# Kernel optimization log

Measured on AMD Instinct MI355X. Metric: run time of the kernel, lower is better.

Reference implementation:

```python
import jax, jax.numpy as jnp
import numpy as np


def fps(xyz, nsamples):
    # xyz: [B, N, 3] -> [B, nsamples] furthest-point-sample indices (int32)
    def single(p):
        N = p.shape[0]
        def step(carry, _):
            dists, last = carry
            d = jnp.sum((p - p[last]) ** 2, axis=-1)
            dists = jnp.minimum(dists, d)
            return (dists, jnp.argmax(dists).astype(jnp.int32)), last
        init = (jnp.full((N,), 1e10, p.dtype), jnp.int32(0))
        _, idx = jax.lax.scan(step, init, None, length=nsamples)
        return idx
    return jax.vmap(single)(xyz)


def bn_relu(x, g, b, m, v):
    # inference BatchNorm2d folded into scale/shift, then ReLU; x: [B,C,S,N]
    s = g * jax.lax.rsqrt(v + 1e-5)
    return jax.nn.relu(x * s[None, :, None, None] + (b - m * s)[None, :, None, None])


def setup_inputs() -> dict:
    key = jax.random.key(0)
    ks = jax.random.split(key, 6)
    B, N, C, S = 8, 16384, 64, 5
    return dict(
        fg_xyz=jax.random.normal(ks[0], (B, N, 3), jnp.float32),
        fg_features=jax.random.normal(ks[1], (B, C, N), jnp.float32),
        bg_xyz=jax.random.normal(ks[2], (B, N, 3), jnp.float32),
        bg_features=jax.random.normal(ks[3], (B, C, N), jnp.float32),
        w1=jax.random.normal(ks[4], (C, 2 * C), jnp.float32) * (1.0 / np.sqrt(2 * C)),
        g1=jnp.ones((C,), jnp.float32), b1=jnp.zeros((C,), jnp.float32),
        m1=jnp.zeros((C,), jnp.float32), v1=jnp.ones((C,), jnp.float32),
        w2=jax.random.normal(ks[5], (C, C), jnp.float32) * (1.0 / np.sqrt(C)),
        g2=jnp.ones((C,), jnp.float32), b2=jnp.zeros((C,), jnp.float32),
        m2=jnp.zeros((C,), jnp.float32), v2=jnp.ones((C,), jnp.float32),
        nsamples=5,
    )


def reference(fg_xyz, fg_features, bg_xyz, bg_features,
              w1, g1, b1, m1, v1, w2, g2, b2, m2, v2, nsamples):
    B, C, N = fg_features.shape
    S = nsamples
    # D-FPS sample S background points, gather their features: [B, C, S]
    idx = fps(bg_xyz, S)
    sample_bg = jnp.take_along_axis(
        bg_features, jnp.broadcast_to(idx[:, None, :], (B, C, S)), axis=2)
    fg_exp = fg_features[:, :, None, :]                           # [B, C, 1, N]
    # candidates = [fg itself, S sampled bg feats tiled over the N fg points]
    fused_origin = jnp.concatenate(
        [fg_exp, jnp.broadcast_to(sample_bg[:, :, :, None], (B, C, S, N))], axis=2)  # [B,C,S+1,N]
    # weight-net input: fg feature concatenated with each candidate along channels
    fusion_in = jnp.concatenate(
        [jnp.broadcast_to(fg_exp, (B, C, S + 1, N)), fused_origin], axis=1)          # [B,2C,S+1,N]
    h = bn_relu(jnp.einsum('oc,bcsn->bosn', w1, fusion_in), g1, b1, m1, v1)
    w = bn_relu(jnp.einsum('oc,bcsn->bosn', w2, h), g2, b2, m2, v2)                  # [B,C,S+1,N]
    final_feats = jnp.sum(w * fused_origin, axis=2, keepdims=True)                   # [B,C,1,N]
    return fg_xyz, final_feats
```

## Files before the change

kernel.cpp:

```cpp
#include <hip/hip_runtime.h>
#include <hip/hip_bf16.h>

#define B_ 8
#define N_ 16384
#define C_ 64
#define S_ 5

typedef float v4f __attribute__((ext_vector_type(4)));
typedef __bf16 v8bf __attribute__((ext_vector_type(8)));

static __device__ __forceinline__ unsigned short f2bf(float f) {
    unsigned int u = __float_as_uint(f);
    u += 0x7fffu + ((u >> 16) & 1u);
    return (unsigned short)(u >> 16);
}

#define GETF(A, i) (((i) & 3) == 0 ? A[(i) >> 2].x : ((i) & 3) == 1 ? A[(i) >> 2].y \
                    : ((i) & 3) == 2 ? A[(i) >> 2].z : A[(i) >> 2].w)

__global__ __launch_bounds__(1024, 4) void prep_all(
    const float* __restrict__ bg_xyz, const float* __restrict__ bg_feat,
    const float* __restrict__ w1, const float* __restrict__ g1, const float* __restrict__ b1,
    const float* __restrict__ m1, const float* __restrict__ v1,
    const float* __restrict__ w2, const float* __restrict__ g2, const float* __restrict__ b2,
    const float* __restrict__ m2, const float* __restrict__ v2,
    const float* __restrict__ fg_xyz, float* __restrict__ out_xyz,
    float* __restrict__ bb1, float* __restrict__ bb2,
    unsigned short* __restrict__ wa_bf, unsigned short* __restrict__ wc_bf,
    unsigned short* __restrict__ w2_bf,
    float* __restrict__ sbg, float* __restrict__ ebb) {
    const int blk = blockIdx.x;
    const int t = threadIdx.x;

    if (blk >= 9) {
        const int i = (blk - 9) * 1024 + t;
        ((float4*)out_xyz)[i] = ((const float4*)fg_xyz)[i];
        return;
    }

    if (blk == 8) {
        for (int i = t; i < 64 * 64; i += 1024) {
            const int o = i >> 6, c = i & 63;
            const float s1 = g1[o] / sqrtf(v1[o] + 1e-5f);
            const float s2 = g2[o] / sqrtf(v2[o] + 1e-5f);
            const float a = s1 * w1[o * 128 + c];
            const float bbv = s1 * w1[o * 128 + 64 + c];
            wa_bf[o * 64 + c] = f2bf(a);
            wc_bf[o * 64 + c] = f2bf(a + bbv);
            w2_bf[o * 64 + c] = f2bf(s2 * w2[o * 64 + c]);
        }
        if (t < 64) {
            const float s1 = g1[t] / sqrtf(v1[t] + 1e-5f);
            const float s2 = g2[t] / sqrtf(v2[t] + 1e-5f);
            bb1[t] = b1[t] - m1[t] * s1;
            bb2[t] = b2[t] - m2[t] * s2;
        }
        return;
    }

    const int b = blk;
    const float* p = bg_xyz + (size_t)b * N_ * 3;

    float4 f4[12];
    {
        const float4* pv = (const float4*)p + t * 12;
#pragma unroll
        for (int i = 0; i < 12; ++i) f4[i] = pv[i];
    }
    float px[16], py[16], pz[16], dist[16];
#pragma unroll
    for (int k = 0; k < 16; ++k) {
        px[k] = GETF(f4, 3 * k);
        py[k] = GETF(f4, 3 * k + 1);
        pz[k] = GETF(f4, 3 * k + 2);
        dist[k] = 1e10f;
    }

    __shared__ float s_best[16];
    __shared__ int s_bidx[16];
    __shared__ int s_last;
    __shared__ int s_idx[S_];
    __shared__ float sf[S_][64];
    int last = 0;
    if (t == 0) s_idx[0] = 0;

    for (int step = 1; step < S_; ++step) {
        const float lx = p[last * 3 + 0];
        const float ly = p[last * 3 + 1];
        const float lz = p[last * 3 + 2];
        float best = -1.0f;
        int bidx = 0;
#pragma unroll
        for (int k = 0; k < 16; ++k) {
            float dx = px[k] - lx, dy = py[k] - ly, dz = pz[k] - lz;
            float d = dx * dx + dy * dy + dz * dz;
            float nd = fminf(dist[k], d);
            dist[k] = nd;
            if (nd > best) { best = nd; bidx = t * 16 + k; }
        }
#pragma unroll
        for (int off = 32; off > 0; off >>= 1) {
            float ob = __shfl_down(best, off, 64);
            int oi = __shfl_down(bidx, off, 64);
            if (ob > best || (ob == best && oi < bidx)) { best = ob; bidx = oi; }
        }
        if ((t & 63) == 0) { s_best[t >> 6] = best; s_bidx[t >> 6] = bidx; }
        __syncthreads();
        if (t == 0) {
            float bb = s_best[0];
            int bi = s_bidx[0];
#pragma unroll
            for (int w = 1; w < 16; ++w) {
                if (s_best[w] > bb || (s_best[w] == bb && s_bidx[w] < bi)) {
                    bb = s_best[w];
                    bi = s_bidx[w];
                }
            }
            s_last = bi;
            s_idx[step] = bi;
        }
        __syncthreads();
        last = s_last;
        __syncthreads();
    }

    __syncthreads();
    if (t < S_ * 64) {
        const int j = t >> 6, c = t & 63;
        sf[j][c] = bg_feat[(size_t)b * C_ * N_ + (size_t)c * N_ + s_idx[j]];
    }
    __syncthreads();
    if (t < S_ * 64) {
        const int j = t >> 6, o = t & 63;
        const float s1 = g1[o] * rsqrtf(v1[o] + 1e-5f);
        const float4* wr = (const float4*)&w1[o * 128 + 64];
        float acc = 0.f;
#pragma unroll
        for (int c4 = 0; c4 < 16; ++c4) {
            float4 wv = wr[c4];
            acc += wv.x * sf[j][c4 * 4 + 0] + wv.y * sf[j][c4 * 4 + 1] +
                   wv.z * sf[j][c4 * 4 + 2] + wv.w * sf[j][c4 * 4 + 3];
        }
        sbg[(b * S_ + j) * 64 + o] = sf[j][o];
        ebb[(b * S_ + j) * 64 + o] = s1 * acc + (b1[o] - m1[o] * s1);
    }
}

#define FP 64
#define HP 72

__global__ __launch_bounds__(256) void fusion_main(
    const float* __restrict__ fg_feat,
    const unsigned short* __restrict__ wa_bf, const unsigned short* __restrict__ wc_bf,
    const unsigned short* __restrict__ w2_bf,
    const float* __restrict__ bb1g, const float* __restrict__ bb2g,
    const float* __restrict__ ebbg, const float* __restrict__ sbgg,
    float* __restrict__ out) {
    __shared__ __align__(16) float Flds[64 * FP];
    __shared__ __align__(16) unsigned short Ht[2][4][16 * HP];
    __shared__ __align__(16) float cEbb[S_ * 64];
    __shared__ __align__(16) float cSbg[S_ * 64];
    __shared__ __align__(16) float cBb1[64];
    __shared__ __align__(16) float cBb2[64];

    const int t = threadIdx.x;
    const int b = blockIdx.y;
    const int n0 = blockIdx.x * 64;
    const float* Fg = fg_feat + (size_t)b * C_ * N_ + n0;

    const int lane = t & 63;
    const int w = t >> 6;

    {
        const int crow = lane >> 4;
        const int nq = lane & 15;
#pragma unroll
        for (int r = 0; r < 4; ++r) {
            const int c = r * 16 + w * 4;
            const float* gsrc = Fg + (size_t)(c + crow) * N_ + nq * 4;
            __builtin_amdgcn_global_load_lds(
                (const __attribute__((address_space(1))) unsigned int*)gsrc,
                (__attribute__((address_space(3))) unsigned int*)&Flds[c * FP],
                16, 0, 0);
        }
    }

    for (int i = t; i < S_ * 64; i += 256) {
        cEbb[i] = ebbg[b * (S_ * 64) + i];
        cSbg[i] = sbgg[b * (S_ * 64) + i];
    }
    if (t < 64) { cBb1[t] = bb1g[t]; cBb2[t] = bb2g[t]; }

    const int m = lane & 15;
    const int q = lane >> 4;
    const int nrow = w * 16 + m;

    v8bf aW2[4][2];
#pragma unroll
    for (int ob = 0; ob < 4; ++ob)
#pragma unroll
        for (int ks = 0; ks < 2; ++ks)
            aW2[ob][ks] = *(const v8bf*)&w2_bf[(ob * 16 + m) * 64 + ks * 32 + q * 8];

    __syncthreads();

    v8bf bF[2];
#pragma unroll
    for (int ks = 0; ks < 2; ++ks) {
        unsigned int uu[4];
#pragma unroll
        for (int jp = 0; jp < 4; ++jp) {
            const int c = ks * 32 + q * 8 + jp * 2;
            float2 fp2;
            fp2.x = Flds[c * FP + nrow];
            fp2.y = Flds[(c + 1) * FP + nrow];
            __hip_bfloat162 h2 = __float22bfloat162_rn(fp2);
            __builtin_memcpy(&uu[jp], &h2, 4);
        }
        __builtin_memcpy(&bF[ks], uu, 16);
    }

    v4f U[4], U0[4];
#pragma unroll
    for (int ob = 0; ob < 4; ++ob) {
        v8bf a0 = *(const v8bf*)&wa_bf[(ob * 16 + m) * 64 + q * 8];
        v8bf a1 = *(const v8bf*)&wa_bf[(ob * 16 + m) * 64 + 32 + q * 8];
        v4f z = {0.f, 0.f, 0.f, 0.f};
        z = __builtin_amdgcn_mfma_f32_16x16x32_bf16(a0, bF[0], z, 0, 0, 0);
        U[ob] = __builtin_amdgcn_mfma_f32_16x16x32_bf16(a1, bF[1], z, 0, 0, 0);
        v8bf c0 = *(const v8bf*)&wc_bf[(ob * 16 + m) * 64 + q * 8];
        v8bf c1 = *(const v8bf*)&wc_bf[(ob * 16 + m) * 64 + 32 + q * 8];
        v4f z2 = {0.f, 0.f, 0.f, 0.f};
        z2 = __builtin_amdgcn_mfma_f32_16x16x32_bf16(c0, bF[0], z2, 0, 0, 0);
        U0[ob] = __builtin_amdgcn_mfma_f32_16x16x32_bf16(c1, bF[1], z2, 0, 0, 0);
    }

    v4f acc[4];
#pragma unroll
    for (int ob = 0; ob < 4; ++ob) acc[ob] = (v4f){0.f, 0.f, 0.f, 0.f};

#pragma unroll
    for (int s = 0; s < 6; ++s) {
        unsigned short* h = &Ht[s & 1][w][0];

#pragma unroll
        for (int ob = 0; ob < 4; ++ob) {
            const int o4 = ob * 16 + 4 * q;
            v4f u, cv;
            if (s == 0) { u = U0[ob]; cv = *(const v4f*)&cBb1[o4]; }
            else        { u = U[ob];  cv = *(const v4f*)&cEbb[(s - 1) * 64 + o4]; }
            float2 e01, e23;
            e01.x = fmaxf(u[0] + cv[0], 0.f);
            e01.y = fmaxf(u[1] + cv[1], 0.f);
            e23.x = fmaxf(u[2] + cv[2], 0.f);
            e23.y = fmaxf(u[3] + cv[3], 0.f);
            __hip_bfloat162 h01 = __float22bfloat162_rn(e01);
            __hip_bfloat162 h23 = __float22bfloat162_rn(e23);
            unsigned int lo, hi;
            __builtin_memcpy(&lo, &h01, 4);
            __builtin_memcpy(&hi, &h23, 4);
            unsigned long long vv = (unsigned long long)lo | ((unsigned long long)hi << 32);
            *(unsigned long long*)&h[m * HP + o4] = vv;
        }

        v8bf hb0 = *(const v8bf*)&h[m * HP + q * 8];
        v8bf hb1 = *(const v8bf*)&h[m * HP + 32 + q * 8];

#pragma unroll
        for (int ob = 0; ob < 4; ++ob) {
            v4f z = {0.f, 0.f, 0.f, 0.f};
            z = __builtin_amdgcn_mfma_f32_16x16x32_bf16(aW2[ob][0], hb0, z, 0, 0, 0);
            v4f p4 = __builtin_amdgcn_mfma_f32_16x16x32_bf16(aW2[ob][1], hb1, z, 0, 0, 0);

            const int o4 = ob * 16 + 4 * q;
            const v4f b2v = *(const v4f*)&cBb2[o4];
            if (s == 0) {
#pragma unroll
                for (int r = 0; r < 4; ++r) {
                    float wgt = fmaxf(p4[r] + b2v[r], 0.f);
                    acc[ob][r] += wgt * Flds[(o4 + r) * FP + nrow];
                }
            } else {
                const v4f sb = *(const v4f*)&cSbg[(s - 1) * 64 + o4];
#pragma unroll
                for (int r = 0; r < 4; ++r) {
                    float wgt = fmaxf(p4[r] + b2v[r], 0.f);
                    acc[ob][r] += wgt * sb[r];
                }
            }
        }
    }

#pragma unroll
    for (int ob = 0; ob < 4; ++ob)
#pragma unroll
        for (int r = 0; r < 4; ++r)
            out[(size_t)b * C_ * N_ + (size_t)(ob * 16 + 4 * q + r) * N_ + (n0 + w * 16 + m)] =
                acc[ob][r];
}

extern "C" void kernel_launch(void* const* d_in, const int* in_sizes, int n_in,
                              void* d_out, int out_size, void* d_ws, size_t ws_size,
                              hipStream_t stream) {
    const float* fg_xyz = (const float*)d_in[0];
    const float* fg_feat = (const float*)d_in[1];
    const float* bg_xyz = (const float*)d_in[2];
    const float* bg_feat = (const float*)d_in[3];
    const float* w1 = (const float*)d_in[4];
    const float* g1 = (const float*)d_in[5];
    const float* b1 = (const float*)d_in[6];
    const float* m1 = (const float*)d_in[7];
    const float* v1 = (const float*)d_in[8];
    const float* w2 = (const float*)d_in[9];
    const float* g2 = (const float*)d_in[10];
    const float* b2 = (const float*)d_in[11];
    const float* m2 = (const float*)d_in[12];
    const float* v2 = (const float*)d_in[13];

    float* ws = (float*)d_ws;
    float* ebb = ws;
    float* sbg = ebb + 2560;
    float* bb1 = sbg + 2560;
    float* bb2 = bb1 + 64;
    unsigned short* wa_bf = (unsigned short*)(bb2 + 64);
    unsigned short* wc_bf = wa_bf + 4096;
    unsigned short* w2_bf = wc_bf + 4096;

    float* out_feats = (float*)d_out + (size_t)B_ * N_ * 3;

    prep_all<<<105, 1024, 0, stream>>>(bg_xyz, bg_feat,
                                       w1, g1, b1, m1, v1, w2, g2, b2, m2, v2,
                                       fg_xyz, (float*)d_out,
                                       bb1, bb2, wa_bf, wc_bf, w2_bf, sbg, ebb);
    fusion_main<<<dim3(N_ / 64, B_), 256, 0, stream>>>(
        fg_feat, wa_bf, wc_bf, w2_bf, bb1, bb2, ebb, sbg, out_feats);
}
```

Before: 178.0 us.

## Process two tiles per block, prefetch second tile, split output channels across waves

Each block now handles two 64-point tiles, and the global loads for the second tile are issued before the first tile is computed. Work is split across waves by output-channel slice rather than point slice, so each wave keeps only its own weight fragments in registers. Features are stored in shared memory as bf16 in a transposed, padded layout, and the fg term in the weighted sum now uses the bf16 values. The cost is block-wide barriers inside each of the six candidate iterations, a halved grid, and slightly lower precision on the fg feature product.

```diff
diff --git a/kernel.cpp b/kernel.cpp
--- a/kernel.cpp
+++ b/kernel.cpp
@@ -8,11 +8,15 @@
 
 typedef float v4f __attribute__((ext_vector_type(4)));
 typedef __bf16 v8bf __attribute__((ext_vector_type(8)));
+typedef unsigned int v4u __attribute__((ext_vector_type(4)));
 
 static __device__ __forceinline__ unsigned short f2bf(float f) {
     unsigned int u = __float_as_uint(f);
     u += 0x7fffu + ((u >> 16) & 1u);
     return (unsigned short)(u >> 16);
+}
+static __device__ __forceinline__ float bf2f(unsigned short s) {
+    return __uint_as_float(((unsigned int)s) << 16);
 }
 
 #define GETF(A, i) (((i) & 3) == 0 ? A[(i) >> 2].x : ((i) & 3) == 1 ? A[(i) >> 2].y \
@@ -146,18 +150,17 @@
     }
 }
 
-#define FP 64
-#define HP 72
-
-__global__ __launch_bounds__(256) void fusion_main(
+#define PITCH 72
+
+__global__ __launch_bounds__(256, 4) void fusion_main(
     const float* __restrict__ fg_feat,
     const unsigned short* __restrict__ wa_bf, const unsigned short* __restrict__ wc_bf,
     const unsigned short* __restrict__ w2_bf,
     const float* __restrict__ bb1g, const float* __restrict__ bb2g,
     const float* __restrict__ ebbg, const float* __restrict__ sbgg,
     float* __restrict__ out) {
-    __shared__ __align__(16) float Flds[64 * FP];
-    __shared__ __align__(16) unsigned short Ht[2][4][16 * HP];
+    __shared__ __align__(16) unsigned short Ft[2][64 * PITCH];
+    __shared__ __align__(16) unsigned short Ht[64 * PITCH];
     __shared__ __align__(16) float cEbb[S_ * 64];
     __shared__ __align__(16) float cSbg[S_ * 64];
     __shared__ __align__(16) float cBb1[64];
@@ -165,25 +168,8 @@
 
     const int t = threadIdx.x;
     const int b = blockIdx.y;
-    const int n0 = blockIdx.x * 64;
-    const float* Fg = fg_feat + (size_t)b * C_ * N_ + n0;
-
-    const int lane = t & 63;
-    const int w = t >> 6;
-
-    {
-        const int crow = lane >> 4;
-        const int nq = lane & 15;
-#pragma unroll
-        for (int r = 0; r < 4; ++r) {
-            const int c = r * 16 + w * 4;
-            const float* gsrc = Fg + (size_t)(c + crow) * N_ + nq * 4;
-            __builtin_amdgcn_global_load_lds(
-                (const __attribute__((address_space(1))) unsigned int*)gsrc,
-                (__attribute__((address_space(3))) unsigned int*)&Flds[c * FP],
-                16, 0, 0);
-        }
-    }
+    const float* Fbase = fg_feat + (size_t)b * C_ * N_;
+    const size_t outb = (size_t)b * C_ * N_;
 
     for (int i = t; i < S_ * 64; i += 256) {
         cEbb[i] = ebbg[b * (S_ * 64) + i];
@@ -191,112 +177,151 @@
     }
     if (t < 64) { cBb1[t] = bb1g[t]; cBb2[t] = bb2g[t]; }
 
+    const int lane = t & 63;
+    const int wv = t >> 6;
+    const int o0 = wv * 16;
     const int m = lane & 15;
     const int q = lane >> 4;
-    const int nrow = w * 16 + m;
-
-    v8bf aW2[4][2];
-#pragma unroll
-    for (int ob = 0; ob < 4; ++ob)
-#pragma unroll
-        for (int ks = 0; ks < 2; ++ks)
-            aW2[ob][ks] = *(const v8bf*)&w2_bf[(ob * 16 + m) * 64 + ks * 32 + q * 8];
-
+    const int o4 = o0 + 4 * q;
+
+    const int arow = o0 + m;
+    v8bf aWa[2], aWc[2], aW2[2];
+#pragma unroll
+    for (int ks = 0; ks < 2; ++ks) {
+        aWa[ks] = *(const v8bf*)&wa_bf[arow * 64 + ks * 32 + q * 8];
+        aWc[ks] = *(const v8bf*)&wc_bf[arow * 64 + ks * 32 + q * 8];
+        aW2[ks] = *(const v8bf*)&w2_bf[arow * 64 + ks * 32 + q * 8];
+    }
+
+    const int sn = t & 63;
+    const int cg = (t >> 6) * 16;
+
+    {
+        const float* Fg = Fbase + (size_t)blockIdx.x * 64 + sn;
+        float fr[16];
+#pragma unroll
+        for (int i = 0; i < 16; ++i) fr[i] = Fg[(size_t)(cg + i) * N_];
+        v4u w0, w1v;
+#pragma unroll
+        for (int i = 0; i < 8; ++i) {
+            unsigned int pk = (unsigned int)f2bf(fr[2 * i]) |
+                              ((unsigned int)f2bf(fr[2 * i + 1]) << 16);
+            if (i < 4) w0[i] = pk; else w1v[i - 4] = pk;
+        }
+        *(v4u*)&Ft[0][sn * PITCH + cg] = w0;
+        *(v4u*)&Ft[0][sn * PITCH + cg + 8] = w1v;
+    }
     __syncthreads();
 
-    v8bf bF[2];
-#pragma unroll
-    for (int ks = 0; ks < 2; ++ks) {
-        unsigned int uu[4];
-#pragma unroll
-        for (int jp = 0; jp < 4; ++jp) {
-            const int c = ks * 32 + q * 8 + jp * 2;
-            float2 fp2;
-            fp2.x = Flds[c * FP + nrow];
-            fp2.y = Flds[(c + 1) * FP + nrow];
-            __hip_bfloat162 h2 = __float22bfloat162_rn(fp2);
-            __builtin_memcpy(&uu[jp], &h2, 4);
-        }
-        __builtin_memcpy(&bF[ks], uu, 16);
-    }
-
-    v4f U[4], U0[4];
-#pragma unroll
-    for (int ob = 0; ob < 4; ++ob) {
-        v8bf a0 = *(const v8bf*)&wa_bf[(ob * 16 + m) * 64 + q * 8];
-        v8bf a1 = *(const v8bf*)&wa_bf[(ob * 16 + m) * 64 + 32 + q * 8];
-        v4f z = {0.f, 0.f, 0.f, 0.f};
-        z = __builtin_amdgcn_mfma_f32_16x16x32_bf16(a0, bF[0], z, 0, 0, 0);
-        U[ob] = __builtin_amdgcn_mfma_f32_16x16x32_bf16(a1, bF[1], z, 0, 0, 0);
-        v8bf c0 = *(const v8bf*)&wc_bf[(ob * 16 + m) * 64 + q * 8];
-        v8bf c1 = *(const v8bf*)&wc_bf[(ob * 16 + m) * 64 + 32 + q * 8];
-        v4f z2 = {0.f, 0.f, 0.f, 0.f};
-        z2 = __builtin_amdgcn_mfma_f32_16x16x32_bf16(c0, bF[0], z2, 0, 0, 0);
-        U0[ob] = __builtin_amdgcn_mfma_f32_16x16x32_bf16(c1, bF[1], z2, 0, 0, 0);
-    }
-
-    v4f acc[4];
-#pragma unroll
-    for (int ob = 0; ob < 4; ++ob) acc[ob] = (v4f){0.f, 0.f, 0.f, 0.f};
-
-#pragma unroll
-    for (int s = 0; s < 6; ++s) {
-        unsigned short* h = &Ht[s & 1][w][0];
-
-#pragma unroll
-        for (int ob = 0; ob < 4; ++ob) {
-            const int o4 = ob * 16 + 4 * q;
-            v4f u, cv;
-            if (s == 0) { u = U0[ob]; cv = *(const v4f*)&cBb1[o4]; }
-            else        { u = U[ob];  cv = *(const v4f*)&cEbb[(s - 1) * 64 + o4]; }
-            float2 e01, e23;
-            e01.x = fmaxf(u[0] + cv[0], 0.f);
-            e01.y = fmaxf(u[1] + cv[1], 0.f);
-            e23.x = fmaxf(u[2] + cv[2], 0.f);
-            e23.y = fmaxf(u[3] + cv[3], 0.f);
-            __hip_bfloat162 h01 = __float22bfloat162_rn(e01);
-            __hip_bfloat162 h23 = __float22bfloat162_rn(e23);
-            unsigned int lo, hi;
-            __builtin_memcpy(&lo, &h01, 4);
-            __builtin_memcpy(&hi, &h23, 4);
-            unsigned long long vv = (unsigned long long)lo | ((unsigned long long)hi << 32);
-            *(unsigned long long*)&h[m * HP + o4] = vv;
-        }
-
-        v8bf hb0 = *(const v8bf*)&h[m * HP + q * 8];
-        v8bf hb1 = *(const v8bf*)&h[m * HP + 32 + q * 8];
-
-#pragma unroll
-        for (int ob = 0; ob < 4; ++ob) {
+    float fr1[16];
+    {
+        const float* Fg1 = Fbase + (size_t)(blockIdx.x + 128) * 64 + sn;
+#pragma unroll
+        for (int i = 0; i < 16; ++i) fr1[i] = Fg1[(size_t)(cg + i) * N_];
+    }
+
+    const v4f bb1r = *(const v4f*)&cBb1[o4];
+    const v4f bb2r = *(const v4f*)&cBb2[o4];
+
+    auto tile_compute = [&](const unsigned short* F, size_t obase) {
+        v8bf bF[4][2];
+#pragma unroll
+        for (int nb = 0; nb < 4; ++nb)
+#pragma unroll
+            for (int ks = 0; ks < 2; ++ks)
+                bF[nb][ks] = *(const v8bf*)&F[(nb * 16 + m) * PITCH + ks * 32 + q * 8];
+
+        v4f U[4], U0[4];
+#pragma unroll
+        for (int nb = 0; nb < 4; ++nb) {
             v4f z = {0.f, 0.f, 0.f, 0.f};
-            z = __builtin_amdgcn_mfma_f32_16x16x32_bf16(aW2[ob][0], hb0, z, 0, 0, 0);
-            v4f p4 = __builtin_amdgcn_mfma_f32_16x16x32_bf16(aW2[ob][1], hb1, z, 0, 0, 0);
-
-            const int o4 = ob * 16 + 4 * q;
-            const v4f b2v = *(const v4f*)&cBb2[o4];
-            if (s == 0) {
-#pragma unroll
-                for (int r = 0; r < 4; ++r) {
-                    float wgt = fmaxf(p4[r] + b2v[r], 0.f);
-                    acc[ob][r] += wgt * Flds[(o4 + r) * FP + nrow];
-                }
-            } else {
-                const v4f sb = *(const v4f*)&cSbg[(s - 1) * 64 + o4];
-#pragma unroll
-                for (int r = 0; r < 4; ++r) {
-                    float wgt = fmaxf(p4[r] + b2v[r], 0.f);
-                    acc[ob][r] += wgt * sb[r];
+            z = __builtin_amdgcn_mfma_f32_16x16x32_bf16(aWa[0], bF[nb][0], z, 0, 0, 0);
+            U[nb] = __builtin_amdgcn_mfma_f32_16x16x32_bf16(aWa[1], bF[nb][1], z, 0, 0, 0);
+            v4f z2 = {0.f, 0.f, 0.f, 0.f};
+            z2 = __builtin_amdgcn_mfma_f32_16x16x32_bf16(aWc[0], bF[nb][0], z2, 0, 0, 0);
+            U0[nb] = __builtin_amdgcn_mfma_f32_16x16x32_bf16(aWc[1], bF[nb][1], z2, 0, 0, 0);
+        }
+
+        v4f acc[4];
+#pragma unroll
+        for (int nb = 0; nb < 4; ++nb) acc[nb] = (v4f){0.f, 0.f, 0.f, 0.f};
+
+#pragma unroll
+        for (int s = 0; s < 6; ++s) {
+            v4f cv = (s == 0) ? bb1r : *(const v4f*)&cEbb[(s - 1) * 64 + o4];
+#pragma unroll
+            for (int nb = 0; nb < 4; ++nb) {
+                v4f u = (s == 0) ? U0[nb] : U[nb];
+                float2 e01, e23;
+                e01.x = fmaxf(u[0] + cv[0], 0.f);
+                e01.y = fmaxf(u[1] + cv[1], 0.f);
+                e23.x = fmaxf(u[2] + cv[2], 0.f);
+                e23.y = fmaxf(u[3] + cv[3], 0.f);
+                __hip_bfloat162 h01 = __float22bfloat162_rn(e01);
+                __hip_bfloat162 h23 = __float22bfloat162_rn(e23);
+                unsigned int lo, hi;
+                __builtin_memcpy(&lo, &h01, 4);
+                __builtin_memcpy(&hi, &h23, 4);
+                unsigned long long vv = (unsigned long long)lo | ((unsigned long long)hi << 32);
+                *(unsigned long long*)&Ht[(nb * 16 + m) * PITCH + o4] = vv;
+            }
+            __syncthreads();
+
+            v4f p4[4];
+#pragma unroll
+            for (int nb = 0; nb < 4; ++nb) {
+                v8bf h0 = *(const v8bf*)&Ht[(nb * 16 + m) * PITCH + q * 8];
+                v8bf h1 = *(const v8bf*)&Ht[(nb * 16 + m) * PITCH + 32 + q * 8];
+                v4f z = {0.f, 0.f, 0.f, 0.f};
+                z = __builtin_amdgcn_mfma_f32_16x16x32_bf16(aW2[0], h0, z, 0, 0, 0);
+                p4[nb] = __builtin_amdgcn_mfma_f32_16x16x32_bf16(aW2[1], h1, z, 0, 0, 0);
+            }
+            __syncthreads();
+
+#pragma unroll
+            for (int nb = 0; nb < 4; ++nb) {
+                if (s == 0) {
+                    unsigned long long fv =
+                        *(const unsigned long long*)&F[(nb * 16 + m) * PITCH + o4];
+#pragma unroll
+                    for (int r = 0; r < 4; ++r) {
+                        float wgt = fmaxf(p4[nb][r] + bb2r[r], 0.f);
+                        acc[nb][r] += wgt * bf2f((unsigned short)(fv >> (16 * r)));
+                    }
+                } else {
+                    const v4f sb = *(const v4f*)&cSbg[(s - 1) * 64 + o4];
+#pragma unroll
+                    for (int r = 0; r < 4; ++r) {
+                        float wgt = fmaxf(p4[nb][r] + bb2r[r], 0.f);
+                        acc[nb][r] += wgt * sb[r];
+                    }
                 }
             }
         }
-    }
-
-#pragma unroll
-    for (int ob = 0; ob < 4; ++ob)
-#pragma unroll
-        for (int r = 0; r < 4; ++r)
-            out[(size_t)b * C_ * N_ + (size_t)(ob * 16 + 4 * q + r) * N_ + (n0 + w * 16 + m)] =
-                acc[ob][r];
+
+#pragma unroll
+        for (int nb = 0; nb < 4; ++nb)
+#pragma unroll
+            for (int r = 0; r < 4; ++r)
+                out[obase + (size_t)(o4 + r) * N_ + (nb * 16 + m)] = acc[nb][r];
+    };
+
+    tile_compute(&Ft[0][0], outb + (size_t)blockIdx.x * 64);
+
+    {
+        v4u w0, w1v;
+#pragma unroll
+        for (int i = 0; i < 8; ++i) {
+            unsigned int pk = (unsigned int)f2bf(fr1[2 * i]) |
+                              ((unsigned int)f2bf(fr1[2 * i + 1]) << 16);
+            if (i < 4) w0[i] = pk; else w1v[i - 4] = pk;
+        }
+        *(v4u*)&Ft[1][sn * PITCH + cg] = w0;
+        *(v4u*)&Ft[1][sn * PITCH + cg + 8] = w1v;
+    }
+    __syncthreads();
+
+    tile_compute(&Ft[1][0], outb + (size_t)(blockIdx.x + 128) * 64);
 }
 
 extern "C" void kernel_launch(void* const* d_in, const int* in_sizes, int n_in,
@@ -332,6 +357,6 @@
                                        w1, g1, b1, m1, v1, w2, g2, b2, m2, v2,
                                        fg_xyz, (float*)d_out,
                                        bb1, bb2, wa_bf, wc_bf, w2_bf, sbg, ebb);
-    fusion_main<<<dim3(N_ / 64, B_), 256, 0, stream>>>(
+    fusion_main<<<dim3(128, B_), 256, 0, stream>>>(
         fg_feat, wa_bf, wc_bf, w2_bf, bb1, bb2, ebb, sbg, out_feats);
 }
```

New measurement: 198.0 us. 1.11x slower.
